# Performance work log

Measured on AMD Instinct MI355X. Metric: run time of the kernel, lower is better.

The kernel has to match this reference:

```python
import jax, jax.numpy as jnp
import numpy as np

B, T, DIM, H = 2, 2048, 512, 8
EPS = 1e-6


def setup_inputs() -> dict:
    key = jax.random.key(0)
    ks = jax.random.split(key, 6)
    scale = 0.05  # keep activations in a sane range for softmax/elu
    return {
        "x": jax.random.normal(ks[0], (B, T, DIM), dtype=jnp.float32),
        "Wq": jax.random.normal(ks[1], (DIM, DIM), dtype=jnp.float32) * scale,
        "Wk": jax.random.normal(ks[2], (DIM, DIM), dtype=jnp.float32) * scale,
        "Wv": jax.random.normal(ks[3], (DIM, DIM), dtype=jnp.float32) * scale,
        "Wo": jax.random.normal(ks[4], (DIM, DIM), dtype=jnp.float32) * scale,
        "bo": jax.random.normal(ks[5], (DIM,), dtype=jnp.float32) * scale,
    }


def reference(x, Wq, Wk, Wv, Wo, bo):
    b, t, dim = x.shape
    h = H
    d = dim // h
    # projections (nn.Linear: x @ W.T)
    q = x @ Wq.T
    k = x @ Wk.T
    v = x @ Wv.T
    mh = lambda z: z.reshape(b, t, h, d).transpose(0, 2, 1, 3)  # [b,h,t,d]
    q, k, v = mh(q), mh(k), mh(v)
    # causal linear attention with buckets = n (bucket size 1, no shift)
    q = jax.nn.softmax(q, axis=-1)
    k = jax.nn.elu(k) + 1.0  # psi
    k_cumsum = jnp.cumsum(k, axis=2)                       # [b,h,t,d]
    context = jnp.einsum('bhnd,bhne->bhnde', k, v)         # per-position outer products
    context = jnp.cumsum(context, axis=2)                  # causal prefix sum, [b,h,t,d,d]
    context = context / (k_cumsum[..., None] + EPS)        # safe_div
    attn = jnp.einsum('bhnd,bhnde->bhne', q, context)      # [b,h,t,d]
    out = attn.transpose(0, 2, 1, 3).reshape(b, t, dim)
    return out @ Wo.T + bo
```

## Files before the change

### kernel.cpp

```cpp
#include <hip/hip_runtime.h>

#define T_SEQ 2048
#define DIMM 512
#define NH 8
#define HD 64
#define BB 2
#define CHUNK 64
#define NCHUNK 32
#define EPSV 1e-6f
#define LDST 72
#define CST2 198

typedef __attribute__((ext_vector_type(8))) short bf16x8;
typedef __attribute__((ext_vector_type(4))) short s16x4;
typedef __attribute__((ext_vector_type(4))) float f32x4;

static __device__ inline short f2bf(float f) {
    union { float f; unsigned u; } v; v.f = f;
    unsigned r = v.u + 0x7FFFu + ((v.u >> 16) & 1u);
    return (short)(r >> 16);
}
static __device__ inline float bf2f(short s) {
    union { unsigned u; float f; } v; v.u = ((unsigned)(unsigned short)s) << 16;
    return v.f;
}
static __device__ __forceinline__ void gload_lds16(const void* g, void* l) {
    __builtin_amdgcn_global_load_lds(
        (__attribute__((address_space(1))) void*)g,
        (__attribute__((address_space(3))) void*)l, 16, 0, 0);
}

__global__ __launch_bounds__(256) void convert_kernel(
    const float* __restrict__ x, const float* __restrict__ Wq,
    const float* __restrict__ Wk, const float* __restrict__ Wv,
    const float* __restrict__ Wo,
    short* __restrict__ xb, short* __restrict__ Wcat, short* __restrict__ Wob)
{
    const int u = blockIdx.x * 256 + threadIdx.x;
    const float* src; short* dst;
    if (u < 262144) {
        src = x + (size_t)u * 8; dst = xb + (size_t)u * 8;
    } else {
        const int v = u - 262144;
        const int o = (v & 32767) * 8;
        if (v < 32768)       { src = Wq + o; dst = Wcat + o; }
        else if (v < 65536)  { src = Wk + o; dst = Wcat + 262144 + o; }
        else if (v < 98304)  { src = Wv + o; dst = Wcat + 524288 + o; }
        else                 { src = Wo + o; dst = Wob + o; }
    }
    const float4 a = *(const float4*)src;
    const float4 b = *(const float4*)(src + 4);
    *(bf16x8*)dst = (bf16x8){f2bf(a.x), f2bf(a.y), f2bf(a.z), f2bf(a.w),
                             f2bf(b.x), f2bf(b.y), f2bf(b.z), f2bf(b.w)};
}

__global__ __launch_bounds__(256) void fusedproj_kernel(
    const short* __restrict__ xb, const short* __restrict__ Wcat,
    short* __restrict__ Qs, short* __restrict__ Kbf,
    short* __restrict__ Ktb, short* __restrict__ Vt,
    float* __restrict__ Schunk, float* __restrict__ kchunk)
{
    __shared__ short S[16384];
    short* As = S;
    short* Bs = S + 4096;
    short* Cs = S;
    const int h = blockIdx.x;
    const int m0 = blockIdx.y * 64;
    const int b = m0 >> 11;
    const int t0 = m0 & (T_SEQ - 1);
    const int c = t0 >> 6;
    const int bh = b * NH + h;
    const int tid = threadIdx.x;
    const int lane = tid & 63, w = tid >> 6;
    const int fr = lane & 15, fg = lane >> 4;
    const int lr = lane >> 3;
    const int sl8 = ((lane & 7) ^ lr) * 8;
    const int xr = fr & 7;
    f32x4 acc[12] = {};

    for (int k0 = 0; k0 < DIMM; k0 += 64) {
        #pragma unroll
        for (int it = 0; it < 2; it++) {
            const int r0 = w * 16 + it * 8;
            gload_lds16(xb + (size_t)(m0 + r0 + lr) * DIMM + k0 + sl8, &As[r0 * 64]);
        }
        #pragma unroll
        for (int it = 0; it < 6; it++) {
            const int rb0 = w * 48 + it * 8;
            const int rb = rb0 + lr;
            const int p = rb >> 6;
            const int gr = p * DIMM + h * 64 + (rb & 63);
            gload_lds16(Wcat + (size_t)gr * DIMM + k0 + sl8, &Bs[rb0 * 64]);
        }
        __syncthreads();
        #pragma unroll
        for (int ks = 0; ks < 2; ks++) {
            const int cc = (((ks << 2) + fg) ^ xr) * 8;
            const bf16x8 af = *(const bf16x8*)&As[(w * 16 + fr) * 64 + cc];
            #pragma unroll
            for (int jj = 0; jj < 12; jj++) {
                const bf16x8 bfr = *(const bf16x8*)&Bs[(jj * 16 + fr) * 64 + cc];
                acc[jj] = __builtin_amdgcn_mfma_f32_16x16x32_bf16(af, bfr, acc[jj], 0, 0, 0);
            }
        }
        __syncthreads();
    }

    #pragma unroll
    for (int jj = 0; jj < 12; jj++)
        #pragma unroll
        for (int reg = 0; reg < 4; reg++) {
            float val = acc[jj][reg];
            if (jj >= 4 && jj < 8) val = (val > 0.f) ? (val + 1.f) : __expf(val);
            Cs[(w * 16 + fg * 4 + reg) * CST2 + jj * 16 + fr] = f2bf(val);
        }
    __syncthreads();

    if (tid < 64) {
        const int r = tid;
        const unsigned* cr = (const unsigned*)&Cs[r * CST2];
        unsigned u[32];
        #pragma unroll
        for (int s = 0; s < 32; s++) u[s] = cr[s];
        float mx = -1e30f;
        #pragma unroll
        for (int s = 0; s < 32; s++) {
            mx = fmaxf(mx, bf2f((short)(u[s] & 0xffff)));
            mx = fmaxf(mx, bf2f((short)(u[s] >> 16)));
        }
        float sum = 0.f;
        #pragma unroll
        for (int s = 0; s < 32; s++) {
            sum += __expf(bf2f((short)(u[s] & 0xffff)) - mx);
            sum += __expf(bf2f((short)(u[s] >> 16)) - mx);
        }
        const float inv = 1.f / sum;
        short* qp = Qs + ((size_t)bh * T_SEQ + t0 + r) * HD;
        #pragma unroll
        for (int g = 0; g < 8; g++) {
            bf16x8 o;
            #pragma unroll
            for (int k = 0; k < 4; k++) {
                const unsigned uv = u[g * 4 + k];
                o[2 * k]     = f2bf(__expf(bf2f((short)(uv & 0xffff)) - mx) * inv);
                o[2 * k + 1] = f2bf(__expf(bf2f((short)(uv >> 16)) - mx) * inv);
            }
            *(bf16x8*)(qp + g * 8) = o;
        }
    } else if (tid < 128) {
        const int r = tid - 64;
        const unsigned* cr = (const unsigned*)&Cs[r * CST2 + 64];
        short* kp = Kbf + ((size_t)bh * T_SEQ + t0 + r) * HD;
        #pragma unroll
        for (int g = 0; g < 8; g++) {
            bf16x8 o;
            #pragma unroll
            for (int k = 0; k < 4; k++) {
                const unsigned uv = cr[g * 4 + k];
                o[2 * k]     = (short)(uv & 0xffff);
                o[2 * k + 1] = (short)(uv >> 16);
            }
            *(bf16x8*)(kp + g * 8) = o;
        }
    }
    {
        const int col = tid & 63, q = tid >> 6;
        short* ktp = Ktb + ((size_t)bh * HD + col) * T_SEQ + t0 + q * 16;
        short* vtp = Vt  + ((size_t)bh * HD + col) * T_SEQ + t0 + q * 16;
        #pragma unroll
        for (int s = 0; s < 2; s++) {
            bf16x8 ok, ov;
            #pragma unroll
            for (int k = 0; k < 8; k++) {
                ok[k] = Cs[(q * 16 + s * 8 + k) * CST2 + 64 + col];
                ov[k] = Cs[(q * 16 + s * 8 + k) * CST2 + 128 + col];
            }
            *(bf16x8*)(ktp + s * 8) = ok;
            *(bf16x8*)(vtp + s * 8) = ov;
        }
    }
    {
        f32x4 a2[4] = {};
        #pragma unroll
        for (int ks = 0; ks < 2; ks++) {
            bf16x8 av;
            #pragma unroll
            for (int uu = 0; uu < 8; uu++)
                av[uu] = Cs[(ks * 32 + fg * 8 + uu) * CST2 + 128 + w * 16 + fr];
            #pragma unroll
            for (int jj = 0; jj < 4; jj++) {
                bf16x8 bk;
                #pragma unroll
                for (int uu = 0; uu < 8; uu++)
                    bk[uu] = Cs[(ks * 32 + fg * 8 + uu) * CST2 + 64 + jj * 16 + fr];
                a2[jj] = __builtin_amdgcn_mfma_f32_16x16x32_bf16(av, bk, a2[jj], 0, 0, 0);
            }
        }
        float* Sout = Schunk + ((size_t)bh * NCHUNK + c) * 4096;
        #pragma unroll
        for (int jj = 0; jj < 4; jj++)
            #pragma unroll
            for (int reg = 0; reg < 4; reg++)
                Sout[(w * 16 + fg * 4 + reg) * 64 + jj * 16 + fr] = a2[jj][reg];
    }
    if (tid < 64) {
        float s = 0.f;
        #pragma unroll
        for (int t = 0; t < 64; t++) s += bf2f(Cs[t * CST2 + 64 + tid]);
        kchunk[((size_t)bh * NCHUNK + c) * 64 + tid] = s;
    }
}

__global__ __launch_bounds__(256) void scan_kernel(float* __restrict__ Schunk,
                                                   float* __restrict__ kchunk)
{
    const int gid = blockIdx.x * 256 + threadIdx.x;
    if (blockIdx.x < 256) {
        const int bh = gid >> 12, i = gid & 4095;
        float run = 0.f;
        float* p = Schunk + (size_t)bh * NCHUNK * 4096 + i;
        for (int c = 0; c < NCHUNK; c++) { const float tv = p[c * 4096]; p[c * 4096] = run; run += tv; }
    } else {
        const int idx = gid - 65536;
        const int bh = idx >> 6, d = idx & 63;
        float run = 0.f;
        float* p = kchunk + (size_t)bh * NCHUNK * 64 + d;
        for (int c = 0; c < NCHUNK; c++) { const float tv = p[c * 64]; p[c * 64] = run; run += tv; }
    }
}

__global__ __launch_bounds__(256) void intra_kernel(
    const short* __restrict__ Qs, const short* __restrict__ Kbf,
    const short* __restrict__ Vt, const float* __restrict__ Schunk,
    const float* __restrict__ kchunk, short* __restrict__ attnb)
{
    __shared__ short B1[64 * LDST];
    __shared__ short B2[64 * LDST];
    __shared__ short KL[64 * LDST];
    __shared__ short VtL[64 * LDST];
    __shared__ short QnL[64 * LDST];
    __shared__ float gsum[4][64];
    __shared__ float kpre[64];
    const int bh = blockIdx.x >> 5, c = blockIdx.x & 31;
    const int tid = threadIdx.x;
    const int lane = tid & 63, w = tid >> 6;
    const int fr = lane & 15, fg = lane >> 4;
    const size_t tdbase = ((size_t)bh * T_SEQ + c * CHUNK) * HD;
    #pragma unroll
    for (int it = 0; it < 2; it++) {
        const int qi = it * 256 + tid;
        const int r = qi >> 3, c8 = (qi & 7) * 8;
        *(bf16x8*)&B1[r * LDST + c8]  = *(const bf16x8*)(Qs + tdbase + r * HD + c8);
        *(bf16x8*)&KL[r * LDST + c8]  = *(const bf16x8*)(Kbf + tdbase + r * HD + c8);
        *(bf16x8*)&VtL[r * LDST + c8] =
            *(const bf16x8*)(Vt + ((size_t)(bh * HD) + r) * T_SEQ + c * CHUNK + c8);
    }
    {
        const float* Sp = Schunk + ((size_t)bh * NCHUNK + c) * 4096;
        #pragma unroll
        for (int it = 0; it < 4; it++) {
            const int qi = it * 256 + tid;
            const int r = qi >> 4, c4 = (qi & 15) * 4;
            const float4 v = *(const float4*)(Sp + r * 64 + c4);
            *(s16x4*)&B2[r * LDST + c4] = (s16x4){f2bf(v.x), f2bf(v.y), f2bf(v.z), f2bf(v.w)};
        }
    }
    if (tid < 64) kpre[tid] = kchunk[((size_t)bh * NCHUNK + c) * 64 + tid];
    __syncthreads();
    {
        float s = 0.f;
        #pragma unroll
        for (int t = 0; t < 16; t++) s += bf2f(KL[(w * 16 + t) * LDST + lane]);
        gsum[w][lane] = s;
    }
    __syncthreads();
    {
        float run = kpre[lane];
        for (int gg = 0; gg < w; gg++) run += gsum[gg][lane];
        #pragma unroll
        for (int t0 = 0; t0 < 16; t0++) {
            const int t = w * 16 + t0;
            run += bf2f(KL[t * LDST + lane]);
            const float qv = bf2f(B1[t * LDST + lane]);
            QnL[t * LDST + lane] = f2bf(qv / (run + EPSV));
        }
    }
    __syncthreads();
    {
        f32x4 a1[4] = {};
        #pragma unroll
        for (int ks = 0; ks < 2; ks++) {
            const bf16x8 aq = *(const bf16x8*)&QnL[(w * 16 + fr) * LDST + ks * 32 + fg * 8];
            #pragma unroll
            for (int j = 0; j < 4; j++) {
                const bf16x8 bk = *(const bf16x8*)&KL[(j * 16 + fr) * LDST + ks * 32 + fg * 8];
                a1[j] = __builtin_amdgcn_mfma_f32_16x16x32_bf16(aq, bk, a1[j], 0, 0, 0);
            }
        }
        const int trow = w * 16 + fg * 4;
        #pragma unroll
        for (int j = 0; j < 4; j++)
            #pragma unroll
            for (int reg = 0; reg < 4; reg++) {
                const int t = trow + reg, s = j * 16 + fr;
                B1[t * LDST + s] = (s <= t) ? f2bf(a1[j][reg]) : (short)0;
            }
    }
    __syncthreads();
    {
        f32x4 a2[4] = {};
        #pragma unroll
        for (int ks = 0; ks < 2; ks++) {
            const bf16x8 aq = *(const bf16x8*)&QnL[(w * 16 + fr) * LDST + ks * 32 + fg * 8];
            const bf16x8 aa = *(const bf16x8*)&B1[(w * 16 + fr) * LDST + ks * 32 + fg * 8];
            #pragma unroll
            for (int j = 0; j < 4; j++) {
                const bf16x8 bs = *(const bf16x8*)&B2[(j * 16 + fr) * LDST + ks * 32 + fg * 8];
                const bf16x8 bv = *(const bf16x8*)&VtL[(j * 16 + fr) * LDST + ks * 32 + fg * 8];
                a2[j] = __builtin_amdgcn_mfma_f32_16x16x32_bf16(aq, bs, a2[j], 0, 0, 0);
                a2[j] = __builtin_amdgcn_mfma_f32_16x16x32_bf16(aa, bv, a2[j], 0, 0, 0);
            }
        }
        short* ap = attnb + tdbase;
        const int trow = w * 16 + fg * 4;
        #pragma unroll
        for (int j = 0; j < 4; j++)
            #pragma unroll
            for (int reg = 0; reg < 4; reg++)
                ap[(trow + reg) * HD + j * 16 + fr] = f2bf(a2[j][reg]);
    }
}

__global__ __launch_bounds__(256) void outproj_mfma_kernel(
    const short* __restrict__ attnb, const short* __restrict__ Wob,
    const float* __restrict__ bo, float* __restrict__ out)
{
    __shared__ short As[64 * 64];
    __shared__ short Bs[64 * 64];
    const int m0 = blockIdx.x * 64;
    const int n0 = blockIdx.y * 64;
    const int tid = threadIdx.x;
    const int lane = tid & 63, w = tid >> 6;
    const int fr = lane & 15, fg = lane >> 4;
    const int lr = lane >> 3, lc = (lane & 7) * 8;
    const int b = m0 >> 11, tbase = m0 & (T_SEQ - 1);
    f32x4 acc[4] = {};
    for (int k0 = 0; k0 < DIMM; k0 += 64) {
        const int h = k0 >> 6;
        #pragma unroll
        for (int it = 0; it < 2; it++) {
            const int r0 = w * 16 + it * 8;
            gload_lds16(attnb + (((size_t)(b * NH + h)) * T_SEQ + tbase + r0 + lr) * HD + lc,
                        &As[r0 * 64]);
            gload_lds16(Wob + (size_t)(n0 + r0 + lr) * DIMM + k0 + lc, &Bs[r0 * 64]);
        }
        __syncthreads();
        #pragma unroll
        for (int ks = 0; ks < 2; ks++) {
            const bf16x8 af = *(const bf16x8*)&As[(w * 16 + fr) * 64 + ks * 32 + fg * 8];
            #pragma unroll
            for (int j = 0; j < 4; j++) {
                const bf16x8 bfr = *(const bf16x8*)&Bs[(j * 16 + fr) * 64 + ks * 32 + fg * 8];
                acc[j] = __builtin_amdgcn_mfma_f32_16x16x32_bf16(af, bfr, acc[j], 0, 0, 0);
            }
        }
        __syncthreads();
    }
    #pragma unroll
    for (int j = 0; j < 4; j++)
        #pragma unroll
        for (int reg = 0; reg < 4; reg++) {
            const int m = m0 + w * 16 + fg * 4 + reg;
            const int n = n0 + j * 16 + fr;
            out[(size_t)m * DIMM + n] = acc[j][reg] + bo[n];
        }
}

extern "C" void kernel_launch(void* const* d_in, const int* in_sizes, int n_in,
                              void* d_out, int out_size, void* d_ws, size_t ws_size,
                              hipStream_t stream)
{
    const float* x  = (const float*)d_in[0];
    const float* Wq = (const float*)d_in[1];
    const float* Wk = (const float*)d_in[2];
    const float* Wv = (const float*)d_in[3];
    const float* Wo = (const float*)d_in[4];
    const float* bo = (const float*)d_in[5];
    float* out = (float*)d_out;

    const size_t NELEM = (size_t)BB * T_SEQ * DIMM;
    short* xb    = (short*)d_ws;
    short* Wcat  = xb + NELEM;
    short* Wob   = Wcat + 786432;
    short* Qs    = Wob + 262144;
    short* Kbf   = Qs + NELEM;
    short* Ktb   = Kbf + NELEM;
    short* Vt    = Ktb + NELEM;
    short* attnb = Vt + NELEM;
    float* Schunk = (float*)(attnb + NELEM);
    float* kchunk = Schunk + (size_t)BB * NH * NCHUNK * 4096;

    convert_kernel<<<dim3(1536), 256, 0, stream>>>(x, Wq, Wk, Wv, Wo, xb, Wcat, Wob);
    fusedproj_kernel<<<dim3(8, 64), 256, 0, stream>>>(xb, Wcat, Qs, Kbf, Ktb, Vt,
                                                      Schunk, kchunk);
    scan_kernel<<<dim3(260), 256, 0, stream>>>(Schunk, kchunk);
    intra_kernel<<<dim3(BB * NH * NCHUNK), 256, 0, stream>>>(Qs, Kbf, Vt, Schunk, kchunk, attnb);
    outproj_mfma_kernel<<<dim3(64, 8), 256, 0, stream>>>(attnb, Wob, bo, out);
}
```

Measured before the change: 56.22 us.

## Split fused QKV projection into standalone GEMM and post-processing kernel

Replaces the fused projection kernel with a generic 64x64-tiled QKV GEMM that writes a bf16 intermediate buffer, followed by a separate kernel that applies the elu+1 transform and the rest of the per-chunk post-processing. This triples the number of GEMM blocks to improve occupancy and load balance. In exchange it adds a full intermediate write and read through global memory, an extra kernel launch, and redundant A-tile loads. It also drops the LDS swizzle, which may cause bank conflicts.

```diff
diff --git a/kernel.cpp b/kernel.cpp
--- a/kernel.cpp
+++ b/kernel.cpp
@@ -10,6 +10,7 @@
 #define EPSV 1e-6f
 #define LDST 72
 #define CST2 198
+#define NC 1536
 
 typedef __attribute__((ext_vector_type(8))) short bf16x8;
 typedef __attribute__((ext_vector_type(4))) short s16x4;
@@ -54,16 +55,52 @@
                              f2bf(b.x), f2bf(b.y), f2bf(b.z), f2bf(b.w)};
 }
 
-__global__ __launch_bounds__(256) void fusedproj_kernel(
+__global__ __launch_bounds__(256) void qkv_gemm_kernel(
     const short* __restrict__ xb, const short* __restrict__ Wcat,
+    short* __restrict__ C)
+{
+    __shared__ short As[64 * 64];
+    __shared__ short Bs[64 * 64];
+    const int m0 = blockIdx.x * 64;
+    const int n0 = blockIdx.y * 64;
+    const int tid = threadIdx.x;
+    const int lane = tid & 63, w = tid >> 6;
+    const int fr = lane & 15, fg = lane >> 4;
+    const int lr = lane >> 3, lc = (lane & 7) * 8;
+    f32x4 acc[4] = {};
+    for (int k0 = 0; k0 < DIMM; k0 += 64) {
+        #pragma unroll
+        for (int it = 0; it < 2; it++) {
+            const int r0 = w * 16 + it * 8;
+            gload_lds16(xb + (size_t)(m0 + r0 + lr) * DIMM + k0 + lc, &As[r0 * 64]);
+            gload_lds16(Wcat + (size_t)(n0 + r0 + lr) * DIMM + k0 + lc, &Bs[r0 * 64]);
+        }
+        __syncthreads();
+        #pragma unroll
+        for (int ks = 0; ks < 2; ks++) {
+            const bf16x8 af = *(const bf16x8*)&As[(w * 16 + fr) * 64 + ks * 32 + fg * 8];
+            #pragma unroll
+            for (int j = 0; j < 4; j++) {
+                const bf16x8 bfr = *(const bf16x8*)&Bs[(j * 16 + fr) * 64 + ks * 32 + fg * 8];
+                acc[j] = __builtin_amdgcn_mfma_f32_16x16x32_bf16(af, bfr, acc[j], 0, 0, 0);
+            }
+        }
+        __syncthreads();
+    }
+    #pragma unroll
+    for (int j = 0; j < 4; j++)
+        #pragma unroll
+        for (int reg = 0; reg < 4; reg++)
+            C[(size_t)(m0 + w * 16 + fg * 4 + reg) * NC + n0 + j * 16 + fr] = f2bf(acc[j][reg]);
+}
+
+__global__ __launch_bounds__(256) void postproc_kernel(
+    const short* __restrict__ C,
     short* __restrict__ Qs, short* __restrict__ Kbf,
     short* __restrict__ Ktb, short* __restrict__ Vt,
     float* __restrict__ Schunk, float* __restrict__ kchunk)
 {
-    __shared__ short S[16384];
-    short* As = S;
-    short* Bs = S + 4096;
-    short* Cs = S;
+    __shared__ short Cs[64 * CST2];
     const int h = blockIdx.x;
     const int m0 = blockIdx.y * 64;
     const int b = m0 >> 11;
@@ -73,47 +110,26 @@
     const int tid = threadIdx.x;
     const int lane = tid & 63, w = tid >> 6;
     const int fr = lane & 15, fg = lane >> 4;
-    const int lr = lane >> 3;
-    const int sl8 = ((lane & 7) ^ lr) * 8;
-    const int xr = fr & 7;
-    f32x4 acc[12] = {};
-
-    for (int k0 = 0; k0 < DIMM; k0 += 64) {
+
+    #pragma unroll
+    for (int s = 0; s < 3; s++)
         #pragma unroll
         for (int it = 0; it < 2; it++) {
-            const int r0 = w * 16 + it * 8;
-            gload_lds16(xb + (size_t)(m0 + r0 + lr) * DIMM + k0 + sl8, &As[r0 * 64]);
-        }
-        #pragma unroll
-        for (int it = 0; it < 6; it++) {
-            const int rb0 = w * 48 + it * 8;
-            const int rb = rb0 + lr;
-            const int p = rb >> 6;
-            const int gr = p * DIMM + h * 64 + (rb & 63);
-            gload_lds16(Wcat + (size_t)gr * DIMM + k0 + sl8, &Bs[rb0 * 64]);
-        }
-        __syncthreads();
-        #pragma unroll
-        for (int ks = 0; ks < 2; ks++) {
-            const int cc = (((ks << 2) + fg) ^ xr) * 8;
-            const bf16x8 af = *(const bf16x8*)&As[(w * 16 + fr) * 64 + cc];
-            #pragma unroll
-            for (int jj = 0; jj < 12; jj++) {
-                const bf16x8 bfr = *(const bf16x8*)&Bs[(jj * 16 + fr) * 64 + cc];
-                acc[jj] = __builtin_amdgcn_mfma_f32_16x16x32_bf16(af, bfr, acc[jj], 0, 0, 0);
-            }
-        }
-        __syncthreads();
-    }
-
-    #pragma unroll
-    for (int jj = 0; jj < 12; jj++)
-        #pragma unroll
-        for (int reg = 0; reg < 4; reg++) {
-            float val = acc[jj][reg];
-            if (jj >= 4 && jj < 8) val = (val > 0.f) ? (val + 1.f) : __expf(val);
-            Cs[(w * 16 + fg * 4 + reg) * CST2 + jj * 16 + fr] = f2bf(val);
-        }
+            const int idx = it * 256 + tid;
+            const int row = idx >> 3, ch = (idx & 7) * 8;
+            *(bf16x8*)&Cs[row * CST2 + s * 64 + ch] =
+                *(const bf16x8*)(C + (size_t)(m0 + row) * NC + s * 512 + h * 64 + ch);
+        }
+    __syncthreads();
+    {
+        const int row = tid & 63, cb = (tid >> 6) * 16;
+        #pragma unroll
+        for (int it = 0; it < 16; it++) {
+            const int idx = row * CST2 + 64 + cb + it;
+            const float v = bf2f(Cs[idx]);
+            Cs[idx] = f2bf((v > 0.f) ? (v + 1.f) : __expf(v));
+        }
+    }
     __syncthreads();
 
     if (tid < 64) {
@@ -399,10 +415,11 @@
     short* attnb = Vt + NELEM;
     float* Schunk = (float*)(attnb + NELEM);
     float* kchunk = Schunk + (size_t)BB * NH * NCHUNK * 4096;
+    short* Cbuf  = (short*)(kchunk + (size_t)BB * NH * NCHUNK * 64);
 
     convert_kernel<<<dim3(1536), 256, 0, stream>>>(x, Wq, Wk, Wv, Wo, xb, Wcat, Wob);
-    fusedproj_kernel<<<dim3(8, 64), 256, 0, stream>>>(xb, Wcat, Qs, Kbf, Ktb, Vt,
-                                                      Schunk, kchunk);
+    qkv_gemm_kernel<<<dim3(64, 24), 256, 0, stream>>>(xb, Wcat, Cbuf);
+    postproc_kernel<<<dim3(8, 64), 256, 0, stream>>>(Cbuf, Qs, Kbf, Ktb, Vt, Schunk, kchunk);
     scan_kernel<<<dim3(260), 256, 0, stream>>>(Schunk, kchunk);
     intra_kernel<<<dim3(BB * NH * NCHUNK), 256, 0, stream>>>(Qs, Kbf, Vt, Schunk, kchunk, attnb);
     outproj_mfma_kernel<<<dim3(64, 8), 256, 0, stream>>>(attnb, Wob, bo, out);
```

Measured after the change: 65.43 us. +16.4%, slower.
